# Performance work log

Measured on AMD Instinct MI355X. Metric: run time of the kernel, lower is better.

Reference implementation:

```python
import jax, jax.numpy as jnp
import numpy as np

N = 50000      # nodes
E = 800000     # edges (avg degree 16)
NODE = 64      # node_attr_size
EDGE = 16      # edge_attr_size
H = 2          # gat_heads
C = 64         # hidden_size (per-head out channels)
F = H * C      # feature_size = 128
L = 2          # num_gat_layers
K = 10         # num_clusters
EPS = 1e-5
NEG_SLOPE = 0.2


def setup_inputs() -> dict:
    key = jax.random.key(0)
    ks = jax.random.split(key, 16)
    s = 0.05
    inp = {
        "x": jax.random.normal(ks[0], (N, NODE), jnp.float32),
        "edge_index": jax.random.randint(ks[1], (2, E), 0, N, jnp.int64 if jax.config.read('jax_enable_x64') else jnp.int32),
        "edge_attr": jax.random.normal(ks[2], (E, EDGE), jnp.float32),
        # node_feat_proj
        "Wp": jax.random.normal(ks[3], (NODE, F), jnp.float32) * s,
        "bp": jnp.zeros((F,), jnp.float32),
        # per-layer LayerNorm affine params, stacked over layers
        "ln_g": jnp.ones((L, F), jnp.float32),
        "ln_b": jnp.zeros((L, F), jnp.float32),
        # per-layer GATv2Conv params (PyG: lin_l, lin_r with bias, lin_edge no bias, att, out bias)
        "Wl": jax.random.normal(ks[4], (L, F, F), jnp.float32) * s,
        "bl": jnp.zeros((L, F), jnp.float32),
        "Wr": jax.random.normal(ks[5], (L, F, F), jnp.float32) * s,
        "br": jnp.zeros((L, F), jnp.float32),
        "We": jax.random.normal(ks[6], (L, EDGE, F), jnp.float32) * s,
        "att": jax.random.normal(ks[7], (L, H, C), jnp.float32) * s,
        "bout": jnp.zeros((L, F), jnp.float32),
        # classifier
        "Wc": jax.random.normal(ks[8], (F, K), jnp.float32) * s,
        "bc": jnp.zeros((K,), jnp.float32),
    }
    return inp


def _layer_norm(x, g, b):
    mu = jnp.mean(x, axis=-1, keepdims=True)
    var = jnp.var(x, axis=-1, keepdims=True)
    return (x - mu) * jax.lax.rsqrt(var + EPS) * g + b


def _gatv2_conv(x, src, dst, Wl, bl, Wr, br, We, att, bout):
    # x: [N, F] -> out: [N, H*C]
    xl = (x @ Wl + bl).reshape(N, H, C)          # source transform
    xr = (x @ Wr + br).reshape(N, H, C)          # target transform
    ee = (jnp.zeros(0),)  # placeholder, edge emb computed by caller closure
    return xl, xr


def reference(x, edge_index, edge_attr, Wp, bp, ln_g, ln_b, Wl, bl, Wr, br, We, att, bout, Wc, bc):
    src, dst = edge_index[0], edge_index[1]
    h = x @ Wp + bp                                   # [N, F]
    for i in range(L):
        identity = h
        hn = _layer_norm(h, ln_g[i], ln_b[i])
        xl = (hn @ Wl[i] + bl[i]).reshape(N, H, C)    # lin_l(x)  (source side)
        xr = (hn @ Wr[i] + br[i]).reshape(N, H, C)    # lin_r(x)  (target side)
        ee = (edge_attr @ We[i]).reshape(E, H, C)     # lin_edge(edge_attr)
        m = xl[src] + xr[dst] + ee                    # [E, H, C]
        m = jnp.where(m > 0, m, NEG_SLOPE * m)        # LeakyReLU(0.2)
        logits = jnp.einsum('ehc,hc->eh', m, att[i])  # [E, H]
        # segment softmax over incoming edges of each target node
        mx = jax.ops.segment_max(logits, dst, num_segments=N)
        ex = jnp.exp(logits - mx[dst])
        den = jax.ops.segment_sum(ex, dst, num_segments=N)
        alpha = ex / den[dst]                         # [E, H]
        msg = xl[src] * alpha[:, :, None]             # [E, H, C]
        agg = jax.ops.segment_sum(msg, dst, num_segments=N)  # [N, H, C]
        hg = agg.reshape(N, F) + bout[i]
        h = jax.nn.relu(hg) + identity                # relu -> dropout(eval no-op) -> residual add
    node_embeddings = h
    classification_output = h @ Wc + bc               # [N, K]
    return (classification_output, node_embeddings)
```

## Files before the change

kernel.cpp:

```cpp
#include <hip/hip_runtime.h>
#include <math.h>

#define N_NODES 50000
#define N_EDGES 800000
#define FDIM 128
#define KCLS 10

typedef float v2f __attribute__((ext_vector_type(2)));

__device__ __forceinline__ v2f pksplat(float a) { v2f r; r.x = a; r.y = a; return r; }
__device__ __forceinline__ v2f pkfma(v2f a, v2f b, v2f c) { return __builtin_elementwise_fma(a, b, c); }
__device__ __forceinline__ v2f pklrelu(v2f v) {
    v2f z = pksplat(0.f);
    v2f mx = __builtin_elementwise_max(v, z);
    v2f mn = __builtin_elementwise_min(v, z);
    return pkfma(pksplat(0.2f), mn, mx);
}
__device__ __forceinline__ int rfl(int v) { return __builtin_amdgcn_readfirstlane(v); }

__device__ __forceinline__ float half_sum32(float x) {
    int v;
    v = __builtin_amdgcn_update_dpp(0, __float_as_int(x), 0xB1, 0xF, 0xF, true);
    x += __int_as_float(v);
    v = __builtin_amdgcn_update_dpp(0, __float_as_int(x), 0x4E, 0xF, 0xF, true);
    x += __int_as_float(v);
    v = __builtin_amdgcn_update_dpp(0, __float_as_int(x), 0x124, 0xF, 0xF, true);
    x += __int_as_float(v);
    v = __builtin_amdgcn_update_dpp(0, __float_as_int(x), 0x128, 0xF, 0xF, true);
    x += __int_as_float(v);
    v = __builtin_amdgcn_ds_swizzle(__float_as_int(x), 0x401F);
    x += __int_as_float(v);
    return x;
}


__global__ void k_count(const int* __restrict__ dst, int* __restrict__ indeg, int e_total) {
    int e = blockIdx.x * 256 + threadIdx.x;
    if (e < e_total) atomicAdd(&indeg[dst[e]], 1);
}

__global__ __launch_bounds__(1024) void k_scan_block(const int* __restrict__ in, int* __restrict__ excl,
                                                     int* __restrict__ bsum, int n) {
    __shared__ int sh[1024];
    int t = threadIdx.x;
    int g = blockIdx.x * 1024 + t;
    int v = (g < n) ? in[g] : 0;
    sh[t] = v;
    __syncthreads();
    for (int d = 1; d < 1024; d <<= 1) {
        int x = (t >= d) ? sh[t - d] : 0;
        __syncthreads();
        sh[t] += x;
        __syncthreads();
    }
    if (g < n) excl[g] = sh[t] - v;
    if (t == 1023) bsum[blockIdx.x] = sh[t];
}

__global__ void k_scan_small(int* bsum, int nb) {
    if (threadIdx.x == 0 && blockIdx.x == 0) {
        int run = 0;
        for (int i = 0; i < nb; i++) { int v = bsum[i]; bsum[i] = run; run += v; }
    }
}

__global__ __launch_bounds__(1024) void k_scan_add(int* __restrict__ offs, const int* __restrict__ bsum,
                                                   int* __restrict__ cursor, int n, int e_total) {
    int g = blockIdx.x * 1024 + threadIdx.x;
    if (g < n) {
        int v = offs[g] + bsum[blockIdx.x];
        offs[g] = v;
        cursor[g] = v;
    }
    if (g == 0) offs[n] = e_total;
}

__global__ void k_scatter_fused(const int* __restrict__ src, const int* __restrict__ dst,
                                const float* __restrict__ edge_attr,
                                int* __restrict__ cursor, int* __restrict__ ssrc,
                                float* __restrict__ sea, int e_total) {
    int e = blockIdx.x * 256 + threadIdx.x;
    if (e < e_total) {
        int d = dst[e];
        int p = atomicAdd(&cursor[d], 1);
        ssrc[p] = src[e];
        const float4* ea = (const float4*)&edge_attr[(size_t)e * 16];
        float4* out = (float4*)&sea[(size_t)p * 16];
        float4 a = ea[0], b = ea[1], c = ea[2], q = ea[3];
        out[0] = a; out[1] = b; out[2] = c; out[3] = q;
    }
}

__global__ void k_scatter(const int* __restrict__ src, const int* __restrict__ dst,
                          int* __restrict__ cursor, int* __restrict__ seid, int* __restrict__ ssrc, int e_total) {
    int e = blockIdx.x * 256 + threadIdx.x;
    if (e < e_total) {
        int d = dst[e];
        int p = atomicAdd(&cursor[d], 1);
        seid[p] = e;
        ssrc[p] = src[e];
    }
}


__device__ __forceinline__ void gemm_pass(const float* __restrict__ W, const float* __restrict__ bias,
                                          float* __restrict__ shw, const float* __restrict__ shn,
                                          int t, int tr, int tc, float acc[4][4]) {
    float4 b4 = *(const float4*)&bias[tc];
#pragma unroll
    for (int j = 0; j < 4; j++) { acc[j][0] = b4.x; acc[j][1] = b4.y; acc[j][2] = b4.z; acc[j][3] = b4.w; }
    for (int kb = 0; kb < 4; kb++) {
        __syncthreads();
        for (int i = t; i < 1024; i += 256)
            ((float4*)shw)[i] = ((const float4*)W)[kb * 1024 + i];
        __syncthreads();
#pragma unroll 8
        for (int kk = 0; kk < 32; kk++) {
            int k = kb * 32 + kk;
            float4 w4 = *(float4*)&shw[kk * 128 + tc];
#pragma unroll
            for (int j = 0; j < 4; j++) {
                float a = shn[(tr + j) * 128 + k];
                acc[j][0] = fmaf(a, w4.x, acc[j][0]);
                acc[j][1] = fmaf(a, w4.y, acc[j][1]);
                acc[j][2] = fmaf(a, w4.z, acc[j][2]);
                acc[j][3] = fmaf(a, w4.w, acc[j][3]);
            }
        }
    }
}

__device__ __forceinline__ void ln_to_shn(float a0[4][4], const float* __restrict__ lng,
                                          const float* __restrict__ lnb, float* __restrict__ shn,
                                          int tr, int tc) {
    float4 g4 = *(const float4*)&lng[tc];
    float4 b4 = *(const float4*)&lnb[tc];
#pragma unroll
    for (int j = 0; j < 4; j++) {
        float s = (a0[j][0] + a0[j][1]) + (a0[j][2] + a0[j][3]);
        float ss = a0[j][0] * a0[j][0] + a0[j][1] * a0[j][1] + a0[j][2] * a0[j][2] + a0[j][3] * a0[j][3];
        s = half_sum32(s);
        ss = half_sum32(ss);
        float mu = s * (1.f / 128.f);
        float var = ss * (1.f / 128.f) - mu * mu;
        float rs = rsqrtf(var + 1e-5f);
        float4 o;
        o.x = (a0[j][0] - mu) * rs * g4.x + b4.x;
        o.y = (a0[j][1] - mu) * rs * g4.y + b4.y;
        o.z = (a0[j][2] - mu) * rs * g4.z + b4.z;
        o.w = (a0[j][3] - mu) * rs * g4.w + b4.w;
        *(float4*)&shn[(tr + j) * 128 + tc] = o;
    }
}


__global__ __launch_bounds__(256) void k_ln_gemm_first(const float* __restrict__ x, const float* __restrict__ Wp,
                                                       const float* __restrict__ bp,
                                                       const float* __restrict__ lng, const float* __restrict__ lnb,
                                                       const float* __restrict__ Wl, const float* __restrict__ bl,
                                                       const float* __restrict__ Wr, const float* __restrict__ br,
                                                       float* __restrict__ h, float* __restrict__ xl,
                                                       float* __restrict__ xr, int n) {
    __shared__ float shn[4096];
    __shared__ float shw[4096];
    int t = threadIdx.x;
    int row0 = blockIdx.x * 32;
    int nrows = min(32, n - row0);
    int tr = (t >> 5) * 4;
    int tc = (t & 31) * 4;
    float* shx = shn;

    for (int i = t; i < 512; i += 256) {
        int r = i >> 4;
        float4 v = make_float4(0.f, 0.f, 0.f, 0.f);
        if (r < nrows) v = ((const float4*)x)[row0 * 16 + i];
        ((float4*)shx)[i] = v;
    }

    float a0[4][4];
    {
        float4 b4 = *(const float4*)&bp[tc];
#pragma unroll
        for (int j = 0; j < 4; j++) { a0[j][0] = b4.x; a0[j][1] = b4.y; a0[j][2] = b4.z; a0[j][3] = b4.w; }
        for (int kb = 0; kb < 2; kb++) {
            __syncthreads();
            for (int i = t; i < 1024; i += 256)
                ((float4*)shw)[i] = ((const float4*)Wp)[kb * 1024 + i];
            __syncthreads();
#pragma unroll 8
            for (int kk = 0; kk < 32; kk++) {
                int k = kb * 32 + kk;
                float4 w4 = *(float4*)&shw[kk * 128 + tc];
#pragma unroll
                for (int j = 0; j < 4; j++) {
                    float a = shx[(tr + j) * 64 + k];
                    a0[j][0] = fmaf(a, w4.x, a0[j][0]);
                    a0[j][1] = fmaf(a, w4.y, a0[j][1]);
                    a0[j][2] = fmaf(a, w4.z, a0[j][2]);
                    a0[j][3] = fmaf(a, w4.w, a0[j][3]);
                }
            }
        }
    }
    __syncthreads();

#pragma unroll
    for (int j = 0; j < 4; j++) {
        int r = row0 + tr + j;
        if (r < n) *(float4*)&h[r * 128 + tc] = make_float4(a0[j][0], a0[j][1], a0[j][2], a0[j][3]);
    }
    ln_to_shn(a0, lng, lnb, shn, tr, tc);

    float acc[4][4];
    gemm_pass(Wl, bl, shw, shn, t, tr, tc, acc);
#pragma unroll
    for (int j = 0; j < 4; j++) {
        int r = row0 + tr + j;
        if (r < n) *(float4*)&xl[r * 128 + tc] = make_float4(acc[j][0], acc[j][1], acc[j][2], acc[j][3]);
    }
    gemm_pass(Wr, br, shw, shn, t, tr, tc, acc);
#pragma unroll
    for (int j = 0; j < 4; j++) {
        int r = row0 + tr + j;
        if (r < n) *(float4*)&xr[r * 128 + tc] = make_float4(acc[j][0], acc[j][1], acc[j][2], acc[j][3]);
    }
}


__global__ __launch_bounds__(256) void k_ln_gemm(const float* __restrict__ h,
                                                 const float* __restrict__ lng, const float* __restrict__ lnb,
                                                 const float* __restrict__ Wl, const float* __restrict__ bl,
                                                 const float* __restrict__ Wr, const float* __restrict__ br,
                                                 float* __restrict__ xl, float* __restrict__ xr, int n) {
    __shared__ float shn[4096];
    __shared__ float shw[4096];
    int t = threadIdx.x;
    int row0 = blockIdx.x * 32;
    int tr = (t >> 5) * 4;
    int tc = (t & 31) * 4;

    float a0[4][4];
#pragma unroll
    for (int j = 0; j < 4; j++) {
        int r = row0 + tr + j;
        float4 v = make_float4(0.f, 0.f, 0.f, 0.f);
        if (r < n) v = *(const float4*)&h[(size_t)r * 128 + tc];
        a0[j][0] = v.x; a0[j][1] = v.y; a0[j][2] = v.z; a0[j][3] = v.w;
    }
    ln_to_shn(a0, lng, lnb, shn, tr, tc);

    float acc[4][4];
    gemm_pass(Wl, bl, shw, shn, t, tr, tc, acc);
#pragma unroll
    for (int j = 0; j < 4; j++) {
        int r = row0 + tr + j;
        if (r < n) *(float4*)&xl[r * 128 + tc] = make_float4(acc[j][0], acc[j][1], acc[j][2], acc[j][3]);
    }
    gemm_pass(Wr, br, shw, shn, t, tr, tc, acc);
#pragma unroll
    for (int j = 0; j < 4; j++) {
        int r = row0 + tr + j;
        if (r < n) *(float4*)&xr[r * 128 + tc] = make_float4(acc[j][0], acc[j][1], acc[j][2], acc[j][3]);
    }
}


#define AGG_BLOCKS 1280

template <bool SORTED, int G>
__device__ __forceinline__ void grpN(const float* __restrict__ xl_lane, const float* __restrict__ eattr,
                                     const int* __restrict__ seid, const int* __restrict__ ssrc,
                                     int j, v2f xr2, const v2f* we, v2f av,
                                     float& den, v2f& A) {
    v2f lx[G];
    const float* ep[G];
#pragma unroll
    for (int g = 0; g < G; g++) {
        int sn = rfl(ssrc[j + g]);
        lx[g] = *(const v2f*)(xl_lane + sn * 128);
        int r = SORTED ? (j + g) : rfl(seid[j + g]);
        ep[g] = &eattr[(size_t)r * 16];
    }
    v2f v[G];
#pragma unroll
    for (int g = 0; g < G; g++) v[g] = lx[g] + xr2;
#pragma unroll
    for (int k = 0; k < 16; k++) {
#pragma unroll
        for (int g = 0; g < G; g++) v[g] = pkfma(pksplat(ep[g][k]), we[k], v[g]);
    }
    float p[G];
#pragma unroll
    for (int g = 0; g < G; g++) {
        v2f t = pklrelu(v[g]) * av;
        p[g] = t.x + t.y;
    }
#pragma unroll
    for (int g = 0; g < G; g++) p[g] = half_sum32(p[g]);
#pragma unroll
    for (int g = 0; g < G; g++) {
        float wv = __expf(p[g]);
        den += wv;
        A = pkfma(pksplat(wv), lx[g], A);
    }
}

template <bool SORTED>
__global__ __launch_bounds__(256, 5) void k_gat_agg(const float* __restrict__ xl, const float* __restrict__ xr,
                                                    const float* __restrict__ eattr,
                                                    const int* __restrict__ offs,
                                                    const int* __restrict__ seid, const int* __restrict__ ssrc,
                                                    const float* __restrict__ We, const float* __restrict__ att,
                                                    const float* __restrict__ bout,
                                                    const float* __restrict__ hin, float* __restrict__ hout, int n) {
    int wid = threadIdx.x >> 6;
    int lane = threadIdx.x & 63;
    int gwave = blockIdx.x * 4 + wid;
    const int nwaves = AGG_BLOCKS * 4;

    int chb = (lane >> 5) * 64 + (lane & 31) * 2;
    const float* xl_lane = xl + chb;

    v2f we[16];
#pragma unroll
    for (int k = 0; k < 16; k++) we[k] = *(const v2f*)&We[k * 128 + chb];
    v2f av = *(const v2f*)&att[chb];
    v2f bo = *(const v2f*)&bout[chb];

    for (int node = gwave; node < n; node += nwaves) {
        v2f xr2 = *(const v2f*)&xr[node * 128 + chb];
        int s = rfl(offs[node]);
        int e = rfl(offs[node + 1]);
        float den = 0.f;
        v2f A = pksplat(0.f);

        int j = s;
        for (; j + 8 <= e; j += 8)
            grpN<SORTED, 8>(xl_lane, eattr, seid, ssrc, j, xr2, we, av, den, A);
        if (j + 4 <= e) {
            grpN<SORTED, 4>(xl_lane, eattr, seid, ssrc, j, xr2, we, av, den, A);
            j += 4;
        }
        for (; j < e; j++)
            grpN<SORTED, 1>(xl_lane, eattr, seid, ssrc, j, xr2, we, av, den, A);

        float inv = (e > s) ? (1.f / den) : 0.f;
        v2f hg = pkfma(A, pksplat(inv), bo);
        hg = __builtin_elementwise_max(hg, pksplat(0.f));
        v2f hv = *(const v2f*)&hin[node * 128 + chb];
        *(v2f*)&hout[node * 128 + chb] = hv + hg;
    }
}


__global__ __launch_bounds__(256) void k_cls_lite(const float* __restrict__ emb, const float* __restrict__ Wc,
                                                  const float* __restrict__ bc, float* __restrict__ out_cls, int n) {
    int wid = threadIdx.x >> 6;
    int lane = threadIdx.x & 63;
    int node = blockIdx.x * 4 + wid;
    if (node >= n) return;
    float h0 = emb[(size_t)node * 128 + lane];
    float h1 = emb[(size_t)node * 128 + 64 + lane];
    float p[10];
#pragma unroll
    for (int k = 0; k < 10; k++) p[k] = h0 * Wc[lane * 10 + k] + h1 * Wc[(64 + lane) * 10 + k];
#pragma unroll
    for (int o = 32; o; o >>= 1) {
#pragma unroll
        for (int k = 0; k < 10; k++) p[k] += __shfl_xor(p[k], o, 64);
    }
    if (lane == 0) {
#pragma unroll
        for (int k = 0; k < 10; k++) out_cls[(size_t)node * 10 + k] = p[k] + bc[k];
    }
}

extern "C" void kernel_launch(void* const* d_in, const int* in_sizes, int n_in,
                              void* d_out, int out_size, void* d_ws, size_t ws_size,
                              hipStream_t stream) {
    const float* x         = (const float*)d_in[0];
    const int*   edge_idx  = (const int*)d_in[1];
    const float* edge_attr = (const float*)d_in[2];
    const float* Wp        = (const float*)d_in[3];
    const float* bp        = (const float*)d_in[4];
    const float* lng       = (const float*)d_in[5];
    const float* lnb       = (const float*)d_in[6];
    const float* Wl        = (const float*)d_in[7];
    const float* bl        = (const float*)d_in[8];
    const float* Wr        = (const float*)d_in[9];
    const float* br        = (const float*)d_in[10];
    const float* We        = (const float*)d_in[11];
    const float* att       = (const float*)d_in[12];
    const float* bout      = (const float*)d_in[13];
    const float* Wc        = (const float*)d_in[14];
    const float* bc        = (const float*)d_in[15];

    const int N = N_NODES, E = N_EDGES;

    char* w = (char*)d_ws;
    size_t used = 0;
    auto take = [&](size_t bytes) -> void* {
        void* p = (void*)(w + used);
        used += (bytes + 255) & ~(size_t)255;
        return p;
    };
    float* h      = (float*)take((size_t)N * 128 * 4);
    float* xl     = (float*)take((size_t)N * 128 * 4);
    float* xr     = (float*)take((size_t)N * 128 * 4);
    int*   indeg  = (int*)take((size_t)N * 4);
    int*   offs   = (int*)take((size_t)(N + 1) * 4);
    int*   cursor = (int*)take((size_t)N * 4);
    int*   bsum   = (int*)take(64 * 4);
    int*   seid   = (int*)take((size_t)E * 4);
    int*   ssrc   = (int*)take((size_t)E * 4);
    float* sea    = (float*)take((size_t)E * 16 * 4);
    bool sorted_ok = (used <= ws_size);

    float* out_cls = (float*)d_out;
    float* out_emb = (float*)d_out + (size_t)N * KCLS;

    const int* srcArr = edge_idx;
    const int* dstArr = edge_idx + E;

    (void)hipMemsetAsync(indeg, 0, (size_t)N * 4, stream);
    k_count<<<(E + 255) / 256, 256, 0, stream>>>(dstArr, indeg, E);
    int NB = (N + 1023) / 1024;
    k_scan_block<<<NB, 1024, 0, stream>>>(indeg, offs, bsum, N);
    k_scan_small<<<1, 64, 0, stream>>>(bsum, NB);
    k_scan_add<<<NB, 1024, 0, stream>>>(offs, bsum, cursor, N, E);
    if (sorted_ok)
        k_scatter_fused<<<(E + 255) / 256, 256, 0, stream>>>(srcArr, dstArr, edge_attr, cursor, ssrc, sea, E);
    else
        k_scatter<<<(E + 255) / 256, 256, 0, stream>>>(srcArr, dstArr, cursor, seid, ssrc, E);

    k_ln_gemm_first<<<(N + 31) / 32, 256, 0, stream>>>(
        x, Wp, bp, lng, lnb,
        Wl, bl, Wr, br, h, xl, xr, N);
    if (sorted_ok)
        k_gat_agg<true><<<AGG_BLOCKS, 256, 0, stream>>>(
            xl, xr, sea, offs, seid, ssrc, We, att, bout, h, h, N);
    else
        k_gat_agg<false><<<AGG_BLOCKS, 256, 0, stream>>>(
            xl, xr, edge_attr, offs, seid, ssrc, We, att, bout, h, h, N);

    k_ln_gemm<<<(N + 31) / 32, 256, 0, stream>>>(
        h, lng + 128, lnb + 128,
        Wl + (size_t)128 * 128, bl + 128,
        Wr + (size_t)128 * 128, br + 128,
        xl, xr, N);
    if (sorted_ok)
        k_gat_agg<true><<<AGG_BLOCKS, 256, 0, stream>>>(
            xl, xr, sea, offs, seid, ssrc,
            We + 16 * 128, att + 128, bout + 128, h, out_emb, N);
    else
        k_gat_agg<false><<<AGG_BLOCKS, 256, 0, stream>>>(
            xl, xr, edge_attr, offs, seid, ssrc,
            We + 16 * 128, att + 128, bout + 128, h, out_emb, N);

    k_cls_lite<<<(N + 3) / 4, 256, 0, stream>>>(out_emb, Wc, bc, out_cls, N);
}
```

Before: 442.0 us.

## Fuse Wl/Wr GEMMs reading weights directly from global memory, drop LDS weight staging

```diff
diff --git a/kernel.cpp b/kernel.cpp
--- a/kernel.cpp
+++ b/kernel.cpp
@@ -102,33 +102,6 @@
     }
 }
 
-
-__device__ __forceinline__ void gemm_pass(const float* __restrict__ W, const float* __restrict__ bias,
-                                          float* __restrict__ shw, const float* __restrict__ shn,
-                                          int t, int tr, int tc, float acc[4][4]) {
-    float4 b4 = *(const float4*)&bias[tc];
-#pragma unroll
-    for (int j = 0; j < 4; j++) { acc[j][0] = b4.x; acc[j][1] = b4.y; acc[j][2] = b4.z; acc[j][3] = b4.w; }
-    for (int kb = 0; kb < 4; kb++) {
-        __syncthreads();
-        for (int i = t; i < 1024; i += 256)
-            ((float4*)shw)[i] = ((const float4*)W)[kb * 1024 + i];
-        __syncthreads();
-#pragma unroll 8
-        for (int kk = 0; kk < 32; kk++) {
-            int k = kb * 32 + kk;
-            float4 w4 = *(float4*)&shw[kk * 128 + tc];
-#pragma unroll
-            for (int j = 0; j < 4; j++) {
-                float a = shn[(tr + j) * 128 + k];
-                acc[j][0] = fmaf(a, w4.x, acc[j][0]);
-                acc[j][1] = fmaf(a, w4.y, acc[j][1]);
-                acc[j][2] = fmaf(a, w4.z, acc[j][2]);
-                acc[j][3] = fmaf(a, w4.w, acc[j][3]);
-            }
-        }
-    }
-}
 
 __device__ __forceinline__ void ln_to_shn(float a0[4][4], const float* __restrict__ lng,
                                           const float* __restrict__ lnb, float* __restrict__ shn,
@@ -154,15 +127,58 @@
 }
 
 
-__global__ __launch_bounds__(256) void k_ln_gemm_first(const float* __restrict__ x, const float* __restrict__ Wp,
-                                                       const float* __restrict__ bp,
-                                                       const float* __restrict__ lng, const float* __restrict__ lnb,
-                                                       const float* __restrict__ Wl, const float* __restrict__ bl,
-                                                       const float* __restrict__ Wr, const float* __restrict__ br,
-                                                       float* __restrict__ h, float* __restrict__ xl,
-                                                       float* __restrict__ xr, int n) {
+__device__ __forceinline__ void dual_gemm_direct(const float* __restrict__ Wl, const float* __restrict__ bl,
+                                                 const float* __restrict__ Wr, const float* __restrict__ br,
+                                                 const float* __restrict__ shn, int tr, int tc,
+                                                 float accl[4][4], float accr[4][4]) {
+    {
+        float4 bl4 = *(const float4*)&bl[tc];
+        float4 br4 = *(const float4*)&br[tc];
+#pragma unroll
+        for (int j = 0; j < 4; j++) {
+            accl[j][0] = bl4.x; accl[j][1] = bl4.y; accl[j][2] = bl4.z; accl[j][3] = bl4.w;
+            accr[j][0] = br4.x; accr[j][1] = br4.y; accr[j][2] = br4.z; accr[j][3] = br4.w;
+        }
+    }
+    for (int kb = 0; kb < 16; kb++) {
+        float a8[4][8];
+#pragma unroll
+        for (int j = 0; j < 4; j++) {
+            float4 u = *(const float4*)&shn[(tr + j) * 128 + kb * 8];
+            float4 v = *(const float4*)&shn[(tr + j) * 128 + kb * 8 + 4];
+            a8[j][0] = u.x; a8[j][1] = u.y; a8[j][2] = u.z; a8[j][3] = u.w;
+            a8[j][4] = v.x; a8[j][5] = v.y; a8[j][6] = v.z; a8[j][7] = v.w;
+        }
+#pragma unroll
+        for (int kk = 0; kk < 8; kk++) {
+            int k = kb * 8 + kk;
+            float4 wl4 = *(const float4*)&Wl[(size_t)k * 128 + tc];
+            float4 wr4 = *(const float4*)&Wr[(size_t)k * 128 + tc];
+#pragma unroll
+            for (int j = 0; j < 4; j++) {
+                float a = a8[j][kk];
+                accl[j][0] = fmaf(a, wl4.x, accl[j][0]);
+                accl[j][1] = fmaf(a, wl4.y, accl[j][1]);
+                accl[j][2] = fmaf(a, wl4.z, accl[j][2]);
+                accl[j][3] = fmaf(a, wl4.w, accl[j][3]);
+                accr[j][0] = fmaf(a, wr4.x, accr[j][0]);
+                accr[j][1] = fmaf(a, wr4.y, accr[j][1]);
+                accr[j][2] = fmaf(a, wr4.z, accr[j][2]);
+                accr[j][3] = fmaf(a, wr4.w, accr[j][3]);
+            }
+        }
+    }
+}
+
+
+__global__ __launch_bounds__(256, 4) void k_ln_gemm_first(const float* __restrict__ x, const float* __restrict__ Wp,
+                                                          const float* __restrict__ bp,
+                                                          const float* __restrict__ lng, const float* __restrict__ lnb,
+                                                          const float* __restrict__ Wl, const float* __restrict__ bl,
+                                                          const float* __restrict__ Wr, const float* __restrict__ br,
+                                                          float* __restrict__ h, float* __restrict__ xl,
+                                                          float* __restrict__ xr, int n) {
     __shared__ float shn[4096];
-    __shared__ float shw[4096];
     int t = threadIdx.x;
     int row0 = blockIdx.x * 32;
     int nrows = min(32, n - row0);
@@ -176,24 +192,29 @@
         if (r < nrows) v = ((const float4*)x)[row0 * 16 + i];
         ((float4*)shx)[i] = v;
     }
+    __syncthreads();
 
     float a0[4][4];
     {
         float4 b4 = *(const float4*)&bp[tc];
 #pragma unroll
         for (int j = 0; j < 4; j++) { a0[j][0] = b4.x; a0[j][1] = b4.y; a0[j][2] = b4.z; a0[j][3] = b4.w; }
-        for (int kb = 0; kb < 2; kb++) {
-            __syncthreads();
-            for (int i = t; i < 1024; i += 256)
-                ((float4*)shw)[i] = ((const float4*)Wp)[kb * 1024 + i];
-            __syncthreads();
-#pragma unroll 8
-            for (int kk = 0; kk < 32; kk++) {
-                int k = kb * 32 + kk;
-                float4 w4 = *(float4*)&shw[kk * 128 + tc];
+        for (int kb = 0; kb < 8; kb++) {
+            float a8[4][8];
+#pragma unroll
+            for (int j = 0; j < 4; j++) {
+                float4 u = *(const float4*)&shx[(tr + j) * 64 + kb * 8];
+                float4 v = *(const float4*)&shx[(tr + j) * 64 + kb * 8 + 4];
+                a8[j][0] = u.x; a8[j][1] = u.y; a8[j][2] = u.z; a8[j][3] = u.w;
+                a8[j][4] = v.x; a8[j][5] = v.y; a8[j][6] = v.z; a8[j][7] = v.w;
+            }
+#pragma unroll
+            for (int kk = 0; kk < 8; kk++) {
+                int k = kb * 8 + kk;
+                float4 w4 = *(const float4*)&Wp[(size_t)k * 128 + tc];
 #pragma unroll
                 for (int j = 0; j < 4; j++) {
-                    float a = shx[(tr + j) * 64 + k];
+                    float a = a8[j][kk];
                     a0[j][0] = fmaf(a, w4.x, a0[j][0]);
                     a0[j][1] = fmaf(a, w4.y, a0[j][1]);
                     a0[j][2] = fmaf(a, w4.z, a0[j][2]);
@@ -210,30 +231,27 @@
         if (r < n) *(float4*)&h[r * 128 + tc] = make_float4(a0[j][0], a0[j][1], a0[j][2], a0[j][3]);
     }
     ln_to_shn(a0, lng, lnb, shn, tr, tc);
-
-    float acc[4][4];
-    gemm_pass(Wl, bl, shw, shn, t, tr, tc, acc);
+    __syncthreads();
+
+    float accl[4][4], accr[4][4];
+    dual_gemm_direct(Wl, bl, Wr, br, shn, tr, tc, accl, accr);
 #pragma unroll
     for (int j = 0; j < 4; j++) {
         int r = row0 + tr + j;
-        if (r < n) *(float4*)&xl[r * 128 + tc] = make_float4(acc[j][0], acc[j][1], acc[j][2], acc[j][3]);
-    }
-    gemm_pass(Wr, br, shw, shn, t, tr, tc, acc);
-#pragma unroll
-    for (int j = 0; j < 4; j++) {
-        int r = row0 + tr + j;
-        if (r < n) *(float4*)&xr[r * 128 + tc] = make_float4(acc[j][0], acc[j][1], acc[j][2], acc[j][3]);
-    }
-}
-
-
-__global__ __launch_bounds__(256) void k_ln_gemm(const float* __restrict__ h,
-                                                 const float* __restrict__ lng, const float* __restrict__ lnb,
-                                                 const float* __restrict__ Wl, const float* __restrict__ bl,
-                                                 const float* __restrict__ Wr, const float* __restrict__ br,
-                                                 float* __restrict__ xl, float* __restrict__ xr, int n) {
+        if (r < n) {
+            *(float4*)&xl[r * 128 + tc] = make_float4(accl[j][0], accl[j][1], accl[j][2], accl[j][3]);
+            *(float4*)&xr[r * 128 + tc] = make_float4(accr[j][0], accr[j][1], accr[j][2], accr[j][3]);
+        }
+    }
+}
+
+
+__global__ __launch_bounds__(256, 4) void k_ln_gemm(const float* __restrict__ h,
+                                                    const float* __restrict__ lng, const float* __restrict__ lnb,
+                                                    const float* __restrict__ Wl, const float* __restrict__ bl,
+                                                    const float* __restrict__ Wr, const float* __restrict__ br,
+                                                    float* __restrict__ xl, float* __restrict__ xr, int n) {
     __shared__ float shn[4096];
-    __shared__ float shw[4096];
     int t = threadIdx.x;
     int row0 = blockIdx.x * 32;
     int tr = (t >> 5) * 4;
@@ -248,19 +266,17 @@
         a0[j][0] = v.x; a0[j][1] = v.y; a0[j][2] = v.z; a0[j][3] = v.w;
     }
     ln_to_shn(a0, lng, lnb, shn, tr, tc);
-
-    float acc[4][4];
-    gemm_pass(Wl, bl, shw, shn, t, tr, tc, acc);
+    __syncthreads();
+
+    float accl[4][4], accr[4][4];
+    dual_gemm_direct(Wl, bl, Wr, br, shn, tr, tc, accl, accr);
 #pragma unroll
     for (int j = 0; j < 4; j++) {
         int r = row0 + tr + j;
-        if (r < n) *(float4*)&xl[r * 128 + tc] = make_float4(acc[j][0], acc[j][1], acc[j][2], acc[j][3]);
-    }
-    gemm_pass(Wr, br, shw, shn, t, tr, tc, acc);
-#pragma unroll
-    for (int j = 0; j < 4; j++) {
-        int r = row0 + tr + j;
-        if (r < n) *(float4*)&xr[r * 128 + tc] = make_float4(acc[j][0], acc[j][1], acc[j][2], acc[j][3]);
+        if (r < n) {
+            *(float4*)&xl[r * 128 + tc] = make_float4(accl[j][0], accl[j][1], accl[j][2], accl[j][3]);
+            *(float4*)&xr[r * 128 + tc] = make_float4(accr[j][0], accr[j][1], accr[j][2], accr[j][3]);
+        }
     }
 }
 
```

Result: slower. 479.5 us (+8.5%).

## Replace FP32 FMA GEMMs with bf16 MFMA and pre-transposed bf16 weights

Applied to the files above, without the earlier changes.

```diff
diff --git a/kernel.cpp b/kernel.cpp
--- a/kernel.cpp
+++ b/kernel.cpp
@@ -7,6 +7,8 @@
 #define KCLS 10
 
 typedef float v2f __attribute__((ext_vector_type(2)));
+typedef short bf16x8 __attribute__((ext_vector_type(8)));
+typedef float f32x4 __attribute__((ext_vector_type(4)));
 
 __device__ __forceinline__ v2f pksplat(float a) { v2f r; r.x = a; r.y = a; return r; }
 __device__ __forceinline__ v2f pkfma(v2f a, v2f b, v2f c) { return __builtin_elementwise_fma(a, b, c); }
@@ -17,6 +19,12 @@
     return pkfma(pksplat(0.2f), mn, mx);
 }
 __device__ __forceinline__ int rfl(int v) { return __builtin_amdgcn_readfirstlane(v); }
+
+__device__ __forceinline__ unsigned int f2bfu(float f) {
+    unsigned int u = __float_as_uint(f);
+    u += 0x7FFFu + ((u >> 16) & 1u);
+    return u >> 16;
+}
 
 __device__ __forceinline__ float half_sum32(float x) {
     int v;
@@ -103,36 +111,26 @@
 }
 
 
-__device__ __forceinline__ void gemm_pass(const float* __restrict__ W, const float* __restrict__ bias,
-                                          float* __restrict__ shw, const float* __restrict__ shn,
-                                          int t, int tr, int tc, float acc[4][4]) {
-    float4 b4 = *(const float4*)&bias[tc];
-#pragma unroll
-    for (int j = 0; j < 4; j++) { acc[j][0] = b4.x; acc[j][1] = b4.y; acc[j][2] = b4.z; acc[j][3] = b4.w; }
-    for (int kb = 0; kb < 4; kb++) {
-        __syncthreads();
-        for (int i = t; i < 1024; i += 256)
-            ((float4*)shw)[i] = ((const float4*)W)[kb * 1024 + i];
-        __syncthreads();
-#pragma unroll 8
-        for (int kk = 0; kk < 32; kk++) {
-            int k = kb * 32 + kk;
-            float4 w4 = *(float4*)&shw[kk * 128 + tc];
-#pragma unroll
-            for (int j = 0; j < 4; j++) {
-                float a = shn[(tr + j) * 128 + k];
-                acc[j][0] = fmaf(a, w4.x, acc[j][0]);
-                acc[j][1] = fmaf(a, w4.y, acc[j][1]);
-                acc[j][2] = fmaf(a, w4.z, acc[j][2]);
-                acc[j][3] = fmaf(a, w4.w, acc[j][3]);
-            }
-        }
-    }
-}
-
-__device__ __forceinline__ void ln_to_shn(float a0[4][4], const float* __restrict__ lng,
-                                          const float* __restrict__ lnb, float* __restrict__ shn,
-                                          int tr, int tc) {
+__global__ void k_prep_w(const float* __restrict__ Wp, const float* __restrict__ Wl,
+                         const float* __restrict__ Wr,
+                         short* __restrict__ Wpt, short* __restrict__ Wlt, short* __restrict__ Wrt) {
+    int i = blockIdx.x * 256 + threadIdx.x;
+    if (i < 128 * 64) {
+        int nn = i >> 6, k = i & 63;
+        Wpt[i] = (short)f2bfu(Wp[k * 128 + nn]);
+    }
+    if (i < 2 * 128 * 128) {
+        int L = i >> 14, r = i & 16383;
+        int nn = r >> 7, k = r & 127;
+        Wlt[i] = (short)f2bfu(Wl[L * 16384 + k * 128 + nn]);
+        Wrt[i] = (short)f2bfu(Wr[L * 16384 + k * 128 + nn]);
+    }
+}
+
+
+__device__ __forceinline__ void ln_to_shn_bf16(float a0[4][4], const float* __restrict__ lng,
+                                               const float* __restrict__ lnb, short* __restrict__ shn,
+                                               int tr, int tc) {
     float4 g4 = *(const float4*)&lng[tc];
     float4 b4 = *(const float4*)&lnb[tc];
 #pragma unroll
@@ -144,100 +142,128 @@
         float mu = s * (1.f / 128.f);
         float var = ss * (1.f / 128.f) - mu * mu;
         float rs = rsqrtf(var + 1e-5f);
-        float4 o;
-        o.x = (a0[j][0] - mu) * rs * g4.x + b4.x;
-        o.y = (a0[j][1] - mu) * rs * g4.y + b4.y;
-        o.z = (a0[j][2] - mu) * rs * g4.z + b4.z;
-        o.w = (a0[j][3] - mu) * rs * g4.w + b4.w;
-        *(float4*)&shn[(tr + j) * 128 + tc] = o;
-    }
-}
-
-
-__global__ __launch_bounds__(256) void k_ln_gemm_first(const float* __restrict__ x, const float* __restrict__ Wp,
-                                                       const float* __restrict__ bp,
-                                                       const float* __restrict__ lng, const float* __restrict__ lnb,
-                                                       const float* __restrict__ Wl, const float* __restrict__ bl,
-                                                       const float* __restrict__ Wr, const float* __restrict__ br,
-                                                       float* __restrict__ h, float* __restrict__ xl,
-                                                       float* __restrict__ xr, int n) {
-    __shared__ float shn[4096];
-    __shared__ float shw[4096];
+        float ox = (a0[j][0] - mu) * rs * g4.x + b4.x;
+        float oy = (a0[j][1] - mu) * rs * g4.y + b4.y;
+        float oz = (a0[j][2] - mu) * rs * g4.z + b4.z;
+        float ow = (a0[j][3] - mu) * rs * g4.w + b4.w;
+        uint2 pk;
+        pk.x = f2bfu(ox) | (f2bfu(oy) << 16);
+        pk.y = f2bfu(oz) | (f2bfu(ow) << 16);
+        *(uint2*)&shn[(tr + j) * 136 + tc] = pk;
+    }
+}
+
+
+__device__ __forceinline__ void dual_gemm_mfma(const short* __restrict__ shn,
+                                               const short* __restrict__ Wlt, const float* __restrict__ bl,
+                                               const short* __restrict__ Wrt, const float* __restrict__ br,
+                                               float* __restrict__ xl, float* __restrict__ xr,
+                                               int t, int row0, int n) {
+    int w = t >> 6, l = t & 63;
+    int lr = l & 15, lg = l >> 4;
+    const short* Wt = (w & 2) ? Wrt : Wlt;
+    const float* bias = (w & 2) ? br : bl;
+    float* out = (w & 2) ? xr : xl;
+    int mt = w & 1;
+
+    bf16x8 af[4];
+#pragma unroll
+    for (int kb = 0; kb < 4; kb++)
+        af[kb] = *(const bf16x8*)&shn[(mt * 16 + lr) * 136 + kb * 32 + lg * 8];
+
+#pragma unroll
+    for (int n0 = 0; n0 < 8; n0++) {
+        float b = bias[n0 * 16 + lr];
+        f32x4 acc = {b, b, b, b};
+#pragma unroll
+        for (int kb = 0; kb < 4; kb++) {
+            bf16x8 bf = *(const bf16x8*)&Wt[(size_t)(n0 * 16 + lr) * 128 + kb * 32 + lg * 8];
+            acc = __builtin_amdgcn_mfma_f32_16x16x32_bf16(af[kb], bf, acc, 0, 0, 0);
+        }
+#pragma unroll
+        for (int r = 0; r < 4; r++) {
+            int row = row0 + mt * 16 + lg * 4 + r;
+            if (row < n) out[(size_t)row * 128 + n0 * 16 + lr] = acc[r];
+        }
+    }
+}
+
+
+__global__ __launch_bounds__(256, 4) void k_ln_gemm_first(const float* __restrict__ x, const short* __restrict__ Wpt,
+                                                          const float* __restrict__ bp,
+                                                          const float* __restrict__ lng, const float* __restrict__ lnb,
+                                                          const short* __restrict__ Wlt, const float* __restrict__ bl,
+                                                          const short* __restrict__ Wrt, const float* __restrict__ br,
+                                                          float* __restrict__ h, float* __restrict__ xl,
+                                                          float* __restrict__ xr, int n) {
+    __shared__ short shx[32 * 72];
+    __shared__ float sh_h[32 * 132];
+    __shared__ short shn[32 * 136];
     int t = threadIdx.x;
     int row0 = blockIdx.x * 32;
     int nrows = min(32, n - row0);
-    int tr = (t >> 5) * 4;
-    int tc = (t & 31) * 4;
-    float* shx = shn;
-
-    for (int i = t; i < 512; i += 256) {
-        int r = i >> 4;
+
+    for (int c = t; c < 512; c += 256) {
+        int r = c >> 4, c4 = (c & 15) * 4;
         float4 v = make_float4(0.f, 0.f, 0.f, 0.f);
-        if (r < nrows) v = ((const float4*)x)[row0 * 16 + i];
-        ((float4*)shx)[i] = v;
-    }
-
+        if (r < nrows) v = ((const float4*)x)[(size_t)(row0 + r) * 16 + (c & 15)];
+        uint2 pk;
+        pk.x = f2bfu(v.x) | (f2bfu(v.y) << 16);
+        pk.y = f2bfu(v.z) | (f2bfu(v.w) << 16);
+        *(uint2*)&shx[r * 72 + c4] = pk;
+    }
+    __syncthreads();
+
+    {
+        int w = t >> 6, l = t & 63;
+        int lr = l & 15, lg = l >> 4;
+        int mt = w & 1, n0base = (w >> 1) * 4;
+        bf16x8 axf[2];
+#pragma unroll
+        for (int kb = 0; kb < 2; kb++)
+            axf[kb] = *(const bf16x8*)&shx[(mt * 16 + lr) * 72 + kb * 32 + lg * 8];
+#pragma unroll
+        for (int i = 0; i < 4; i++) {
+            int n0 = n0base + i;
+            float b = bp[n0 * 16 + lr];
+            f32x4 acc = {b, b, b, b};
+#pragma unroll
+            for (int kb = 0; kb < 2; kb++) {
+                bf16x8 bf = *(const bf16x8*)&Wpt[(size_t)(n0 * 16 + lr) * 64 + kb * 32 + lg * 8];
+                acc = __builtin_amdgcn_mfma_f32_16x16x32_bf16(axf[kb], bf, acc, 0, 0, 0);
+            }
+#pragma unroll
+            for (int r = 0; r < 4; r++)
+                sh_h[(mt * 16 + lg * 4 + r) * 132 + n0 * 16 + lr] = acc[r];
+        }
+    }
+    __syncthreads();
+
+    int tr = (t >> 5) * 4, tc = (t & 31) * 4;
     float a0[4][4];
-    {
-        float4 b4 = *(const float4*)&bp[tc];
-#pragma unroll
-        for (int j = 0; j < 4; j++) { a0[j][0] = b4.x; a0[j][1] = b4.y; a0[j][2] = b4.z; a0[j][3] = b4.w; }
-        for (int kb = 0; kb < 2; kb++) {
-            __syncthreads();
-            for (int i = t; i < 1024; i += 256)
-                ((float4*)shw)[i] = ((const float4*)Wp)[kb * 1024 + i];
-            __syncthreads();
-#pragma unroll 8
-            for (int kk = 0; kk < 32; kk++) {
-                int k = kb * 32 + kk;
-                float4 w4 = *(float4*)&shw[kk * 128 + tc];
-#pragma unroll
-                for (int j = 0; j < 4; j++) {
-                    float a = shx[(tr + j) * 64 + k];
-                    a0[j][0] = fmaf(a, w4.x, a0[j][0]);
-                    a0[j][1] = fmaf(a, w4.y, a0[j][1]);
-                    a0[j][2] = fmaf(a, w4.z, a0[j][2]);
-                    a0[j][3] = fmaf(a, w4.w, a0[j][3]);
-                }
-            }
-        }
-    }
+#pragma unroll
+    for (int j = 0; j < 4; j++) {
+        float4 v = *(const float4*)&sh_h[(tr + j) * 132 + tc];
+        a0[j][0] = v.x; a0[j][1] = v.y; a0[j][2] = v.z; a0[j][3] = v.w;
+        int r = row0 + tr + j;
+        if (r < n) *(float4*)&h[(size_t)r * 128 + tc] = v;
+    }
+    ln_to_shn_bf16(a0, lng, lnb, shn, tr, tc);
     __syncthreads();
 
-#pragma unroll
-    for (int j = 0; j < 4; j++) {
-        int r = row0 + tr + j;
-        if (r < n) *(float4*)&h[r * 128 + tc] = make_float4(a0[j][0], a0[j][1], a0[j][2], a0[j][3]);
-    }
-    ln_to_shn(a0, lng, lnb, shn, tr, tc);
-
-    float acc[4][4];
-    gemm_pass(Wl, bl, shw, shn, t, tr, tc, acc);
-#pragma unroll
-    for (int j = 0; j < 4; j++) {
-        int r = row0 + tr + j;
-        if (r < n) *(float4*)&xl[r * 128 + tc] = make_float4(acc[j][0], acc[j][1], acc[j][2], acc[j][3]);
-    }
-    gemm_pass(Wr, br, shw, shn, t, tr, tc, acc);
-#pragma unroll
-    for (int j = 0; j < 4; j++) {
-        int r = row0 + tr + j;
-        if (r < n) *(float4*)&xr[r * 128 + tc] = make_float4(acc[j][0], acc[j][1], acc[j][2], acc[j][3]);
-    }
-}
-
-
-__global__ __launch_bounds__(256) void k_ln_gemm(const float* __restrict__ h,
-                                                 const float* __restrict__ lng, const float* __restrict__ lnb,
-                                                 const float* __restrict__ Wl, const float* __restrict__ bl,
-                                                 const float* __restrict__ Wr, const float* __restrict__ br,
-                                                 float* __restrict__ xl, float* __restrict__ xr, int n) {
-    __shared__ float shn[4096];
-    __shared__ float shw[4096];
+    dual_gemm_mfma(shn, Wlt, bl, Wrt, br, xl, xr, t, row0, n);
+}
+
+
+__global__ __launch_bounds__(256, 4) void k_ln_gemm(const float* __restrict__ h,
+                                                    const float* __restrict__ lng, const float* __restrict__ lnb,
+                                                    const short* __restrict__ Wlt, const float* __restrict__ bl,
+                                                    const short* __restrict__ Wrt, const float* __restrict__ br,
+                                                    float* __restrict__ xl, float* __restrict__ xr, int n) {
+    __shared__ short shn[32 * 136];
     int t = threadIdx.x;
     int row0 = blockIdx.x * 32;
-    int tr = (t >> 5) * 4;
-    int tc = (t & 31) * 4;
+    int tr = (t >> 5) * 4, tc = (t & 31) * 4;
 
     float a0[4][4];
 #pragma unroll
@@ -247,21 +273,10 @@
         if (r < n) v = *(const float4*)&h[(size_t)r * 128 + tc];
         a0[j][0] = v.x; a0[j][1] = v.y; a0[j][2] = v.z; a0[j][3] = v.w;
     }
-    ln_to_shn(a0, lng, lnb, shn, tr, tc);
-
-    float acc[4][4];
-    gemm_pass(Wl, bl, shw, shn, t, tr, tc, acc);
-#pragma unroll
-    for (int j = 0; j < 4; j++) {
-        int r = row0 + tr + j;
-        if (r < n) *(float4*)&xl[r * 128 + tc] = make_float4(acc[j][0], acc[j][1], acc[j][2], acc[j][3]);
-    }
-    gemm_pass(Wr, br, shw, shn, t, tr, tc, acc);
-#pragma unroll
-    for (int j = 0; j < 4; j++) {
-        int r = row0 + tr + j;
-        if (r < n) *(float4*)&xr[r * 128 + tc] = make_float4(acc[j][0], acc[j][1], acc[j][2], acc[j][3]);
-    }
+    ln_to_shn_bf16(a0, lng, lnb, shn, tr, tc);
+    __syncthreads();
+
+    dual_gemm_mfma(shn, Wlt, bl, Wrt, br, xl, xr, t, row0, n);
 }
 
 
@@ -413,6 +428,9 @@
     int*   bsum   = (int*)take(64 * 4);
     int*   seid   = (int*)take((size_t)E * 4);
     int*   ssrc   = (int*)take((size_t)E * 4);
+    short* Wpt    = (short*)take((size_t)128 * 64 * 2);
+    short* Wlt    = (short*)take((size_t)2 * 128 * 128 * 2);
+    short* Wrt    = (short*)take((size_t)2 * 128 * 128 * 2);
     float* sea    = (float*)take((size_t)E * 16 * 4);
     bool sorted_ok = (used <= ws_size);
 
@@ -433,9 +451,11 @@
     else
         k_scatter<<<(E + 255) / 256, 256, 0, stream>>>(srcArr, dstArr, cursor, seid, ssrc, E);
 
+    k_prep_w<<<128, 256, 0, stream>>>(Wp, Wl, Wr, Wpt, Wlt, Wrt);
+
     k_ln_gemm_first<<<(N + 31) / 32, 256, 0, stream>>>(
-        x, Wp, bp, lng, lnb,
-        Wl, bl, Wr, br, h, xl, xr, N);
+        x, Wpt, bp, lng, lnb,
+        Wlt, bl, Wrt, br, h, xl, xr, N);
     if (sorted_ok)
         k_gat_agg<true><<<AGG_BLOCKS, 256, 0, stream>>>(
             xl, xr, sea, offs, seid, ssrc, We, att, bout, h, h, N);
@@ -445,8 +465,8 @@
 
     k_ln_gemm<<<(N + 31) / 32, 256, 0, stream>>>(
         h, lng + 128, lnb + 128,
-        Wl + (size_t)128 * 128, bl + 128,
-        Wr + (size_t)128 * 128, br + 128,
+        Wlt + 16384, bl + 128,
+        Wrt + 16384, br + 128,
         xl, xr, N);
     if (sorted_ok)
         k_gat_agg<true><<<AGG_BLOCKS, 256, 0, stream>>>(
```

Result: faster. 390.1 us (median of 3 runs) (-11.8%).
